# Kernel optimization log

Hardware: AMD Instinct MI355X
Metric: run time of the kernel (lower is better)

The kernel has to match this reference:

```python
import jax, jax.numpy as jnp
import numpy as np

B, N = 16, 16          # batch, boxes per image
H, W = 640, 640        # image size
PH, PW = 300, 300      # learned patch size
MIN_AREA = 60.0
MAX_ANG = 20.0 * np.pi / 180.0


def setup_inputs() -> dict:
    key = jax.random.key(0)
    k1, k2, k3 = jax.random.split(key, 3)
    images = jax.random.uniform(k1, (B, H, W, 3), jnp.float32, -1.0, 1.0)
    patch = jax.random.uniform(k2, (PH, PW, 3), jnp.float32, -1.0, 1.0)
    kb1, kb2, kb3 = jax.random.split(k3, 3)
    ymin = jax.random.uniform(kb1, (B, N), jnp.float32, 0.0, H - 220.0)
    xmin = jax.random.uniform(kb2, (B, N), jnp.float32, 0.0, W - 220.0)
    hw = jax.random.uniform(kb3, (B, N, 2), jnp.float32, 100.0, 200.0)
    boxes = jnp.stack([ymin, xmin, ymin + hw[..., 0], xmin + hw[..., 1]], axis=-1)
    scale = jnp.float32(0.4)
    return {"boxes": boxes, "images": images, "patch": patch, "scale": scale}


def _bilinear(img, ys, xs):
    # img [Ph,Pw,3]; ys,xs [H,W] continuous source coords -> [H,W,3]
    Ph, Pw = img.shape[0], img.shape[1]
    y0 = jnp.floor(ys)
    x0 = jnp.floor(xs)
    wy = (ys - y0)[..., None]
    wx = (xs - x0)[..., None]
    y0i = jnp.clip(y0.astype(jnp.int32), 0, Ph - 1)
    y1i = jnp.clip(y0i + 1, 0, Ph - 1)
    x0i = jnp.clip(x0.astype(jnp.int32), 0, Pw - 1)
    x1i = jnp.clip(x0i + 1, 0, Pw - 1)
    v00 = img[y0i, x0i]
    v01 = img[y0i, x1i]
    v10 = img[y1i, x0i]
    v11 = img[y1i, x1i]
    return v00 * (1 - wy) * (1 - wx) + v01 * (1 - wy) * wx + v10 * wy * (1 - wx) + v11 * wy * wx


def _per_image(img, boxes_i, patch, scale, key):
    # random_print_adjust: per-channel affine jitter of the patch
    kw, kb, kloop = jax.random.split(key, 3)
    w = jax.random.normal(kw, (1, 1, 3), jnp.float32) * 0.1 + 0.5
    b = jax.random.normal(kb, (1, 1, 3), jnp.float32) * 0.01
    p = jnp.clip(w * patch + b, -1.0, 1.0)
    # BrightnessMatcher: shift patch mean brightness to match the image
    p = jnp.clip(p + (jnp.mean(img) - jnp.mean(p)), -1.0, 1.0)

    oimg = img
    mask0 = jnp.zeros_like(img)
    yy, xx = jnp.meshgrid(jnp.arange(H, dtype=jnp.float32),
                          jnp.arange(W, dtype=jnp.float32), indexing="ij")

    def step(carry, inp):
        image, mask = carry
        box, kk = inp
        ymin, xmin, ymax, xmax = box[0], box[1], box[2], box[3]
        h = ymax - ymin
        ww = xmax - xmin
        longer = jnp.maximum(h, ww)
        ps = jnp.floor(longer * scale)                       # patch_h == patch_w
        diag = jnp.minimum(jnp.sqrt(2.0).astype(jnp.float32) * ps, jnp.float32(W))
        oy = ymin + h / 2.0
        ox = xmin + ww / 2.0
        y0 = jnp.maximum(oy - diag / 2.0, 0.0)
        x0 = jnp.maximum(ox - diag / 2.0, 0.0)
        y0 = jnp.where(y0 + diag > H, H - diag, y0)
        x0 = jnp.where(x0 + diag > W, W - diag, x0)
        # int casts as in the TF code (values are >= 0, trunc == floor)
        y0i = jnp.floor(y0)
        x0i = jnp.floor(x0)
        phi = jnp.maximum(jnp.floor(ps), 1.0)
        diagi = jnp.floor(diag)
        valid_box = (phi * phi) > MIN_AREA

        k1, k2, k3 = jax.random.split(kk, 3)
        angle = jax.random.uniform(k1, (), jnp.float32, -MAX_ANG, MAX_ANG)

        # inverse warp: output pixel -> padded-patch coords -> resized-patch coords
        u = yy - y0i
        v = xx - x0i
        in_sq = (u >= 0) & (v >= 0) & (u < diagi) & (v < diagi)
        c = (diagi - 1.0) / 2.0
        ca, sa = jnp.cos(angle), jnp.sin(angle)
        su = c + ca * (u - c) - sa * (v - c)
        sv = c + sa * (u - c) + ca * (v - c)
        top = jnp.floor((diagi - phi) / 2.0)   # pad offset (floor top/left)
        py = su - top
        px = sv - top
        valid_src = (py >= 0) & (py <= phi - 1) & (px >= 0) & (px <= phi - 1)
        # resized-patch coords -> original patch coords (bilinear resize, half-pixel)
        sy = (py + 0.5) * (PH / phi) - 0.5
        sx = (px + 0.5) * (PW / phi) - 0.5
        samp = _bilinear(p, sy, sx)                                   # [H,W,3]
        noise = jax.random.uniform(k2, samp.shape, jnp.float32, -0.1, 0.1)
        bright = jax.random.uniform(k3, (), jnp.float32, -0.3, 0.3)
        im = jnp.clip(samp + noise + bright, -1.0, 1.0)
        val = jnp.where(valid_src[..., None], im, -2.0)
        val = jnp.where(val < -1.0, image, val)   # fill with current background
        val = jnp.clip(val, -1.0, 1.0)
        sel = (in_sq & valid_box)[..., None]
        new_image = jnp.where(sel, val, image)
        new_mask = jnp.where(sel, oimg - val, mask)
        return (new_image, new_mask), None

    keys = jax.random.split(kloop, N)
    (img_out, mask_out), _ = jax.lax.scan(step, (img, mask0), (boxes_i, keys))
    return img_out, mask_out


def reference(boxes, images, patch, scale):
    keys = jax.random.split(jax.random.key(42), B)
    img_out, mask_out = jax.vmap(_per_image, in_axes=(0, 0, None, None, 0))(
        images, boxes, patch, scale, keys)
    return img_out, mask_out
```

## Files before the change

kernel.cpp:

```cpp
#include <hip/hip_runtime.h>
#include <stdint.h>
#include <math.h>

#define B_ 16
#define N_ 16
#define H_ 640
#define W_ 640
#define PH_ 300
#define PW_ 300

#define IMG_ELEMS (H_*W_*3)
#define PATCH_ELEMS (PH_*PW_*3)

#define TROWS 16
#define TCOLS 64
#define TILES_Y (H_/TROWS)
#define TILES_X (W_/TCOLS)
#define TILES_PER_IMG (TILES_Y*TILES_X)
#define NTILES (B_*TILES_PER_IMG)

typedef float f32x4 __attribute__((ext_vector_type(4)));

__device__ __forceinline__ uint2 tf2x32(uint32_t k0, uint32_t k1, uint32_t x0, uint32_t x1) {
  uint32_t k2 = k0 ^ k1 ^ 0x1BD11BDAu;
#define TFR(r) x0 += x1; x1 = (x1 << (r)) | (x1 >> (32 - (r))); x1 ^= x0;
  x0 += k0; x1 += k1;
  TFR(13) TFR(15) TFR(26) TFR(6)
  x0 += k1; x1 += k2 + 1u;
  TFR(17) TFR(29) TFR(16) TFR(24)
  x0 += k2; x1 += k0 + 2u;
  TFR(13) TFR(15) TFR(26) TFR(6)
  x0 += k0; x1 += k1 + 3u;
  TFR(17) TFR(29) TFR(16) TFR(24)
  x0 += k1; x1 += k2 + 4u;
  TFR(13) TFR(15) TFR(26) TFR(6)
  x0 += k2; x1 += k0 + 5u;
#undef TFR
  return make_uint2(x0, x1);
}

__device__ __forceinline__ uint32_t rb32(uint32_t k0, uint32_t k1, uint32_t i) {
  uint2 o = tf2x32(k0, k1, 0u, i);
  return o.x ^ o.y;
}

__device__ __forceinline__ float u01f(uint32_t bits) {
  return __uint_as_float((bits >> 9) | 0x3F800000u) - 1.0f;
}

__device__ __forceinline__ float erfinv32(float x) {
  float w = -log1pf(-x * x);
  float p;
  if (w < 5.0f) {
    w = w - 2.5f;
    p = 2.81022636e-08f;
    p = fmaf(p, w, 3.43273939e-07f);
    p = fmaf(p, w, -3.5233877e-06f);
    p = fmaf(p, w, -4.39150654e-06f);
    p = fmaf(p, w, 0.00021858087f);
    p = fmaf(p, w, -0.00125372503f);
    p = fmaf(p, w, -0.00417768164f);
    p = fmaf(p, w, 0.246640727f);
    p = fmaf(p, w, 1.50140941f);
  } else {
    w = sqrtf(w) - 3.0f;
    p = -0.000200214257f;
    p = fmaf(p, w, 0.000100950558f);
    p = fmaf(p, w, 0.00134934322f);
    p = fmaf(p, w, -0.00367342844f);
    p = fmaf(p, w, 0.00573950773f);
    p = fmaf(p, w, -0.0076224613f);
    p = fmaf(p, w, 0.00943887047f);
    p = fmaf(p, w, 1.00167406f);
    p = fmaf(p, w, 2.83297682f);
  }
  return p * x;
}

__device__ __forceinline__ float jnormal(uint32_t bits) {
  float lo = __uint_as_float(0xBF7FFFFFu);
  float span = 1.0f - lo;
  float u = fmaxf(lo, u01f(bits) * span + lo);
  return 1.4142135623730951f * erfinv32(u);
}

__global__ __launch_bounds__(256) void reduce_kernel(
    const float* __restrict__ images, const float* __restrict__ patch,
    double* __restrict__ partials) {
  int b = blockIdx.y, j = blockIdx.x, t = threadIdx.x;
  __shared__ float swb[6];
  if (t < 6) {
    uint2 kb  = tf2x32(0u, 42u, 0u, (uint32_t)b);
    uint2 kw  = tf2x32(kb.x, kb.y, 0u, 0u);
    uint2 kbk = tf2x32(kb.x, kb.y, 0u, 1u);
    swb[t] = (t < 3) ? (jnormal(rb32(kw.x,  kw.y,  (uint32_t)t)) * 0.1f + 0.5f)
                     : (jnormal(rb32(kbk.x, kbk.y, (uint32_t)(t - 3))) * 0.01f);
  }
  __syncthreads();
  const float* img = images + (size_t)b * IMG_ELEMS;
  double s = 0.0;
  for (int i = j * 256 + t; i < IMG_ELEMS; i += 64 * 256) s += (double)img[i];
  float w0 = swb[0], w1 = swb[1], w2 = swb[2];
  float b0 = swb[3], b1 = swb[4], b2 = swb[5];
  double sp = 0.0;
  for (int i = j * 256 + t; i < PATCH_ELEMS; i += 64 * 256) {
    int q = i / 3; int ch = i - q * 3;
    float wv = (ch == 0) ? w0 : ((ch == 1) ? w1 : w2);
    float bv = (ch == 0) ? b0 : ((ch == 1) ? b1 : b2);
    float pv = fminf(fmaxf(wv * patch[i] + bv, -1.0f), 1.0f);
    sp += (double)pv;
  }
  __shared__ double sh[256];
  sh[t] = s; __syncthreads();
  for (int o = 128; o > 0; o >>= 1) { if (t < o) sh[t] += sh[t + o]; __syncthreads(); }
  if (t == 0) partials[((size_t)b * 64 + j) * 2 + 0] = sh[0];
  __syncthreads();
  sh[t] = sp; __syncthreads();
  for (int o = 128; o > 0; o >>= 1) { if (t < o) sh[t] += sh[t + o]; __syncthreads(); }
  if (t == 0) partials[((size_t)b * 64 + j) * 2 + 1] = sh[0];
}

__global__ void setup_finalize_kernel(
    const float* __restrict__ boxes, const float* __restrict__ scale_p,
    const double* __restrict__ partials,
    float* __restrict__ params, float* __restrict__ wb, float* __restrict__ dvals) {
  int t = threadIdx.x;
  if (t < B_) {
    double si = 0.0, sp = 0.0;
    for (int j = 0; j < 64; j++) {
      si += partials[((size_t)t * 64 + j) * 2 + 0];
      sp += partials[((size_t)t * 64 + j) * 2 + 1];
    }
    float mi = (float)(si / (double)IMG_ELEMS);
    float mp = (float)(sp / (double)PATCH_ELEMS);
    dvals[t] = mi - mp;
  }
  if (t >= B_*N_) return;
  int b = t >> 4, n = t & 15;
  uint2 kb = tf2x32(0u, 42u, 0u, (uint32_t)b);
  uint2 kw  = tf2x32(kb.x, kb.y, 0u, 0u);
  uint2 kbk = tf2x32(kb.x, kb.y, 0u, 1u);
  uint2 kl  = tf2x32(kb.x, kb.y, 0u, 2u);
  if (n == 0) {
    wb[b*8+0] = jnormal(rb32(kw.x,  kw.y,  0u)) * 0.1f + 0.5f;
    wb[b*8+1] = jnormal(rb32(kw.x,  kw.y,  1u)) * 0.1f + 0.5f;
    wb[b*8+2] = jnormal(rb32(kw.x,  kw.y,  2u)) * 0.1f + 0.5f;
    wb[b*8+3] = jnormal(rb32(kbk.x, kbk.y, 0u)) * 0.01f;
    wb[b*8+4] = jnormal(rb32(kbk.x, kbk.y, 1u)) * 0.01f;
    wb[b*8+5] = jnormal(rb32(kbk.x, kbk.y, 2u)) * 0.01f;
  }
  uint2 kk = tf2x32(kl.x, kl.y, 0u, (uint32_t)n);
  uint2 k1 = tf2x32(kk.x, kk.y, 0u, 0u);
  uint2 k2 = tf2x32(kk.x, kk.y, 0u, 1u);
  uint2 k3 = tf2x32(kk.x, kk.y, 0u, 2u);
  const float MA = (float)(20.0 * 3.14159265358979323846 / 180.0);
  float angle  = fmaxf(-MA,   u01f(rb32(k1.x, k1.y, 0u)) * (MA - (-MA)) + (-MA));
  float bright = fmaxf(-0.3f, u01f(rb32(k3.x, k3.y, 0u)) * (0.3f - (-0.3f)) + (-0.3f));

  const float* bx = boxes + (size_t)t * 4;
  float ymin = bx[0], xmin = bx[1], ymax = bx[2], xmax = bx[3];
  float sc = scale_p[0];
  float h = ymax - ymin, ww = xmax - xmin;
  float longer = fmaxf(h, ww);
  float ps = floorf(longer * sc);
  float diag = fminf(sqrtf(2.0f) * ps, (float)W_);
  float oy = ymin + h * 0.5f;
  float ox = xmin + ww * 0.5f;
  float y0 = fmaxf(oy - diag * 0.5f, 0.0f);
  float x0 = fmaxf(ox - diag * 0.5f, 0.0f);
  if (y0 + diag > (float)H_) y0 = (float)H_ - diag;
  if (x0 + diag > (float)W_) x0 = (float)W_ - diag;
  float y0i = floorf(y0), x0i = floorf(x0);
  float phi = fmaxf(floorf(ps), 1.0f);
  float diagi = floorf(diag);
  float validf = ((phi * phi) > 60.0f) ? 1.0f : 0.0f;
  float c = (diagi - 1.0f) * 0.5f;
  float top = floorf((diagi - phi) * 0.5f);

  float* P = params + t * 16;
  P[0] = y0i; P[1] = x0i; P[2] = diagi; P[3] = phi;
  P[4] = c;
  P[5] = (float)cos((double)angle);
  P[6] = (float)sin((double)angle);
  P[7] = top;
  P[8] = bright; P[9] = (float)PH_ / phi; P[10] = 0.0f; P[11] = validf;
  P[12] = __uint_as_float(k2.x); P[13] = __uint_as_float(k2.y); P[14] = 0.0f; P[15] = 0.0f;
}

__global__ __launch_bounds__(256) void main_kernel(
    const float* __restrict__ images, const float* __restrict__ patch,
    const float* __restrict__ params, const float* __restrict__ wb,
    const float* __restrict__ dvals, float* __restrict__ out) {
  __shared__ float sP[N_ * 16];
  __shared__ float sWB[6];
  __shared__ int sList[N_];
  __shared__ int sCount;
  __shared__ float sT[TROWS * 192];

  int bid = blockIdx.x;
  int b  = (bid & 7) * 2 + ((bid >> 3) & 1);
  int tl = bid >> 4;
  int ty = tl / TILES_X;
  int tx = tl - ty * TILES_X;
  int tid = threadIdx.x;

  if (tid < N_ * 16) sP[tid] = params[b * N_ * 16 + tid];
  if (tid < 6) sWB[tid] = wb[b * 8 + tid];
  if (tid == 0) {
    const float* Pb = params + b * N_ * 16;
    float ys = (float)(ty * TROWS), ye = (float)(ty * TROWS + TROWS - 1);
    float xs = (float)(tx * TCOLS), xe = (float)(tx * TCOLS + TCOLS - 1);
    int cnt = 0;
    for (int n = 0; n < N_; n++) {
      const float* P = Pb + n * 16;
      if (P[11] == 0.0f) continue;
      float last = P[2] - 1.0f;
      if (P[0] + last < ys || P[0] > ye) continue;
      if (P[1] + last < xs || P[1] > xe) continue;
      sList[cnt++] = n;
    }
    sCount = cnt;
  }
  __syncthreads();

  int lane = tid & 63;
  int wv   = tid >> 6;
  size_t ibase = (size_t)b * IMG_ELEMS;
  size_t moff  = (size_t)B_ * IMG_ELEMS;

  int   ck[3], lrk[3];
  size_t fbk[3];
#pragma unroll
  for (int k = 0; k < 3; k++) {
    int t4 = k * 64 + lane;
    int r  = t4 / 48;
    int c  = t4 - r * 48;
    int lr = wv * 4 + r;
    ck[k] = c; lrk[k] = lr;
    fbk[k] = ibase + ((size_t)(ty * TROWS + lr) * W_ + tx * TCOLS) * 3 + (size_t)c * 4;
  }

  if (sCount == 0) {
    const f32x4 z = {0.0f, 0.0f, 0.0f, 0.0f};
#pragma unroll
    for (int k = 0; k < 3; k++) {
      f32x4 d = *(const f32x4*)(images + fbk[k]);
      *(f32x4*)(out + fbk[k]) = d;
      *(f32x4*)(out + moff + fbk[k]) = z;
    }
    return;
  }

  float dsh = dvals[b];

#pragma unroll
  for (int k = 0; k < 3; k++) {
    f32x4 d = *(const f32x4*)(images + fbk[k]);
    *(f32x4*)(&sT[lrk[k] * 192 + ck[k] * 4]) = d;
  }

  int   pj[4];  float yfj[4];
  float xf = (float)(tx * TCOLS + lane);
#pragma unroll
  for (int j = 0; j < 4; j++) {
    int row = ty * TROWS + wv * 4 + j;
    pj[j]  = row * W_ + tx * TCOLS + lane;
    yfj[j] = (float)row;
  }

  float orig[12], img[12], mkv[12];
#pragma unroll
  for (int j = 0; j < 4; j++) {
    int base = (wv * 4 + j) * 192 + lane * 3;
    orig[j*3+0] = sT[base + 0];
    orig[j*3+1] = sT[base + 1];
    orig[j*3+2] = sT[base + 2];
  }
#pragma unroll
  for (int e = 0; e < 12; e++) { img[e] = orig[e]; mkv[e] = 0.0f; }

  int cnt = sCount;
  for (int li = 0; li < cnt; li++) {
    const float* P = sP + sList[li] * 16;
    float P0 = P[0], P1 = P[1], diagi = P[2];
    float phi = P[3], c = P[4], ca = P[5], sa = P[6], top = P[7], bright = P[8], sph = P[9];
    uint32_t k2a = __float_as_uint(P[12]);
    uint32_t k2b = __float_as_uint(P[13]);
    float v = xf - P1;
    bool vok = (v >= 0.0f && v < diagi);
    float t2 = v - c;
#pragma unroll
    for (int j = 0; j < 4; j++) {
      float u = yfj[j] - P0;
      if (!(u >= 0.0f && u < diagi)) continue;
      if (!vok) continue;
      float t1 = u - c;
      float su = (c + ca * t1) - sa * t2;
      float sv = (c + sa * t1) + ca * t2;
      float py = su - top;
      float px = sv - top;
      bool vsrc = (py >= 0.0f) && (py <= phi - 1.0f) && (px >= 0.0f) && (px <= phi - 1.0f);
      if (vsrc) {
        float sy = (py + 0.5f) * sph - 0.5f;
        float sx = (px + 0.5f) * sph - 0.5f;
        float fy = floorf(sy), fx = floorf(sx);
        float wy = sy - fy, wxv = sx - fx;
        int iy0 = min(max((int)fy, 0), PH_ - 1);
        int iy1 = min(iy0 + 1, PH_ - 1);
        int ix0 = min(max((int)fx, 0), PW_ - 1);
        int ix1 = min(ix0 + 1, PW_ - 1);
        int o00 = (iy0 * PW_ + ix0) * 3;
        int o01 = (iy0 * PW_ + ix1) * 3;
        int o10 = (iy1 * PW_ + ix0) * 3;
        int o11 = (iy1 * PW_ + ix1) * 3;
        float omwy = 1.0f - wy, omwx = 1.0f - wxv;
        int nbase = pj[j] * 3;
#pragma unroll
        for (int ch = 0; ch < 3; ch++) {
          float wv2 = sWB[ch], bv = sWB[3 + ch];
          float a00 = fminf(fmaxf(wv2 * patch[o00 + ch] + bv, -1.0f), 1.0f);
          float a01 = fminf(fmaxf(wv2 * patch[o01 + ch] + bv, -1.0f), 1.0f);
          float a10 = fminf(fmaxf(wv2 * patch[o10 + ch] + bv, -1.0f), 1.0f);
          float a11 = fminf(fmaxf(wv2 * patch[o11 + ch] + bv, -1.0f), 1.0f);
          a00 = fminf(fmaxf(a00 + dsh, -1.0f), 1.0f);
          a01 = fminf(fmaxf(a01 + dsh, -1.0f), 1.0f);
          a10 = fminf(fmaxf(a10 + dsh, -1.0f), 1.0f);
          a11 = fminf(fmaxf(a11 + dsh, -1.0f), 1.0f);
          float samp = ((a00 * omwy) * omwx) + ((a01 * omwy) * wxv)
                     + ((a10 * wy) * omwx) + ((a11 * wy) * wxv);
          uint32_t bits = rb32(k2a, k2b, (uint32_t)(nbase + ch));
          float nz = fmaxf(-0.1f, u01f(bits) * (0.1f - (-0.1f)) + (-0.1f));
          float imv = fminf(fmaxf((samp + nz) + bright, -1.0f), 1.0f);
          img[j * 3 + ch] = imv;
          mkv[j * 3 + ch] = orig[j * 3 + ch] - imv;
        }
      } else {
#pragma unroll
        for (int ch = 0; ch < 3; ch++) mkv[j * 3 + ch] = orig[j * 3 + ch] - img[j * 3 + ch];
      }
    }
  }

#pragma unroll
  for (int j = 0; j < 4; j++) {
    int base = (wv * 4 + j) * 192 + lane * 3;
    sT[base + 0] = img[j*3+0];
    sT[base + 1] = img[j*3+1];
    sT[base + 2] = img[j*3+2];
  }
#pragma unroll
  for (int k = 0; k < 3; k++) {
    f32x4 d = *(const f32x4*)(&sT[lrk[k] * 192 + ck[k] * 4]);
    *(f32x4*)(out + fbk[k]) = d;
  }
#pragma unroll
  for (int j = 0; j < 4; j++) {
    int base = (wv * 4 + j) * 192 + lane * 3;
    sT[base + 0] = mkv[j*3+0];
    sT[base + 1] = mkv[j*3+1];
    sT[base + 2] = mkv[j*3+2];
  }
#pragma unroll
  for (int k = 0; k < 3; k++) {
    f32x4 d = *(const f32x4*)(&sT[lrk[k] * 192 + ck[k] * 4]);
    *(f32x4*)(out + moff + fbk[k]) = d;
  }
}

extern "C" void kernel_launch(void* const* d_in, const int* in_sizes, int n_in,
                              void* d_out, int out_size, void* d_ws, size_t ws_size,
                              hipStream_t stream) {
  const float* boxes  = (const float*)d_in[0];
  const float* images = (const float*)d_in[1];
  const float* patch  = (const float*)d_in[2];
  const float* scale  = (const float*)d_in[3];
  float* out = (float*)d_out;

  float* params = (float*)d_ws;
  float* wb     = params + B_ * N_ * 16;
  float* dvals  = wb + B_ * 8;
  double* partials = (double*)((char*)d_ws + 20480);

  reduce_kernel<<<dim3(64, B_), 256, 0, stream>>>(images, patch, partials);
  setup_finalize_kernel<<<1, 256, 0, stream>>>(boxes, scale, partials, params, wb, dvals);
  main_kernel<<<NTILES, 256, 0, stream>>>(images, patch, params, wb, dvals, out);
}
```

Before: 292.0 us.

## Make main kernel persistent and cull boxes per tile with a wave ballot

The main kernel now launches a fixed grid of 2048 blocks, and each block loops over tiles with a grid stride instead of handling exactly one tile. The stride is a multiple of 16, so a block keeps the same image and loads its parameters once. The serial per-tile box-overlap scan on thread 0, with its shared list, is replaced by a parallel test: each lane checks one box and a wave ballot builds a 16-bit overlap mask, which is walked with ctz. This removes the serial culling and block launch/setup overhead, at the cost of possible load imbalance because tiles differ in how many boxes touch them.

```diff
diff --git a/kernel.cpp b/kernel.cpp
--- a/kernel.cpp
+++ b/kernel.cpp
@@ -18,6 +18,7 @@
 #define TILES_X (W_/TCOLS)
 #define TILES_PER_IMG (TILES_Y*TILES_X)
 #define NTILES (B_*TILES_PER_IMG)
+#define MAIN_GRID 2048
 
 typedef float f32x4 __attribute__((ext_vector_type(4)));
 
@@ -193,177 +194,176 @@
     const float* __restrict__ dvals, float* __restrict__ out) {
   __shared__ float sP[N_ * 16];
   __shared__ float sWB[6];
-  __shared__ int sList[N_];
-  __shared__ int sCount;
   __shared__ float sT[TROWS * 192];
 
   int bid = blockIdx.x;
   int b  = (bid & 7) * 2 + ((bid >> 3) & 1);
-  int tl = bid >> 4;
-  int ty = tl / TILES_X;
-  int tx = tl - ty * TILES_X;
   int tid = threadIdx.x;
 
   if (tid < N_ * 16) sP[tid] = params[b * N_ * 16 + tid];
   if (tid < 6) sWB[tid] = wb[b * 8 + tid];
-  if (tid == 0) {
-    const float* Pb = params + b * N_ * 16;
-    float ys = (float)(ty * TROWS), ye = (float)(ty * TROWS + TROWS - 1);
-    float xs = (float)(tx * TCOLS), xe = (float)(tx * TCOLS + TCOLS - 1);
-    int cnt = 0;
-    for (int n = 0; n < N_; n++) {
-      const float* P = Pb + n * 16;
-      if (P[11] == 0.0f) continue;
-      float last = P[2] - 1.0f;
-      if (P[0] + last < ys || P[0] > ye) continue;
-      if (P[1] + last < xs || P[1] > xe) continue;
-      sList[cnt++] = n;
-    }
-    sCount = cnt;
-  }
   __syncthreads();
 
   int lane = tid & 63;
   int wv   = tid >> 6;
   size_t ibase = (size_t)b * IMG_ELEMS;
   size_t moff  = (size_t)B_ * IMG_ELEMS;
-
-  int   ck[3], lrk[3];
-  size_t fbk[3];
+  float dsh = dvals[b];
+
+  int ck[3], lrk[3];
 #pragma unroll
   for (int k = 0; k < 3; k++) {
     int t4 = k * 64 + lane;
     int r  = t4 / 48;
-    int c  = t4 - r * 48;
-    int lr = wv * 4 + r;
-    ck[k] = c; lrk[k] = lr;
-    fbk[k] = ibase + ((size_t)(ty * TROWS + lr) * W_ + tx * TCOLS) * 3 + (size_t)c * 4;
-  }
-
-  if (sCount == 0) {
-    const f32x4 z = {0.0f, 0.0f, 0.0f, 0.0f};
+    ck[k]  = t4 - r * 48;
+    lrk[k] = wv * 4 + r;
+  }
+
+  const float* Pc = sP + (tid & 15) * 16;
+  float cP0 = Pc[0], cP1 = Pc[1], cLast = Pc[2] - 1.0f;
+  bool cValid = (Pc[11] != 0.0f);
+
+  for (int g = bid; g < NTILES; g += MAIN_GRID) {
+    int tl = g >> 4;
+    int ty = tl / TILES_X;
+    int tx = tl - ty * TILES_X;
+
+    float ys = (float)(ty * TROWS), ye = ys + (float)(TROWS - 1);
+    float xs = (float)(tx * TCOLS), xe = xs + (float)(TCOLS - 1);
+    bool hit = cValid && !(cP0 + cLast < ys || cP0 > ye)
+                      && !(cP1 + cLast < xs || cP1 > xe);
+    uint32_t mask = (uint32_t)(__ballot(hit) & 0xFFFFull);
+
+    size_t fbk[3];
+#pragma unroll
+    for (int k = 0; k < 3; k++)
+      fbk[k] = ibase + ((size_t)(ty * TROWS + lrk[k]) * W_ + tx * TCOLS) * 3 + (size_t)ck[k] * 4;
+
+    if (mask == 0u) {
+      const f32x4 z = {0.0f, 0.0f, 0.0f, 0.0f};
+#pragma unroll
+      for (int k = 0; k < 3; k++) {
+        f32x4 d = *(const f32x4*)(images + fbk[k]);
+        *(f32x4*)(out + fbk[k]) = d;
+        *(f32x4*)(out + moff + fbk[k]) = z;
+      }
+      continue;
+    }
+
 #pragma unroll
     for (int k = 0; k < 3; k++) {
       f32x4 d = *(const f32x4*)(images + fbk[k]);
+      *(f32x4*)(&sT[lrk[k] * 192 + ck[k] * 4]) = d;
+    }
+
+    int   pj[4];  float yfj[4];
+    float xf = (float)(tx * TCOLS + lane);
+#pragma unroll
+    for (int j = 0; j < 4; j++) {
+      int row = ty * TROWS + wv * 4 + j;
+      pj[j]  = row * W_ + tx * TCOLS + lane;
+      yfj[j] = (float)row;
+    }
+
+    float orig[12], img[12], mkv[12];
+#pragma unroll
+    for (int j = 0; j < 4; j++) {
+      int base = (wv * 4 + j) * 192 + lane * 3;
+      orig[j*3+0] = sT[base + 0];
+      orig[j*3+1] = sT[base + 1];
+      orig[j*3+2] = sT[base + 2];
+    }
+#pragma unroll
+    for (int e = 0; e < 12; e++) { img[e] = orig[e]; mkv[e] = 0.0f; }
+
+    uint32_t m = mask;
+    while (m) {
+      int n = __builtin_ctz(m);
+      m &= m - 1u;
+      const float* P = sP + n * 16;
+      float P0 = P[0], P1 = P[1], diagi = P[2];
+      float phi = P[3], c = P[4], ca = P[5], sa = P[6], top = P[7], bright = P[8], sph = P[9];
+      uint32_t k2a = __float_as_uint(P[12]);
+      uint32_t k2b = __float_as_uint(P[13]);
+      float v = xf - P1;
+      bool vok = (v >= 0.0f && v < diagi);
+      float t2 = v - c;
+#pragma unroll
+      for (int j = 0; j < 4; j++) {
+        float u = yfj[j] - P0;
+        if (!(u >= 0.0f && u < diagi)) continue;
+        if (!vok) continue;
+        float t1 = u - c;
+        float su = (c + ca * t1) - sa * t2;
+        float sv = (c + sa * t1) + ca * t2;
+        float py = su - top;
+        float px = sv - top;
+        bool vsrc = (py >= 0.0f) && (py <= phi - 1.0f) && (px >= 0.0f) && (px <= phi - 1.0f);
+        if (vsrc) {
+          float sy = (py + 0.5f) * sph - 0.5f;
+          float sx = (px + 0.5f) * sph - 0.5f;
+          float fy = floorf(sy), fx = floorf(sx);
+          float wy = sy - fy, wxv = sx - fx;
+          int iy0 = min(max((int)fy, 0), PH_ - 1);
+          int iy1 = min(iy0 + 1, PH_ - 1);
+          int ix0 = min(max((int)fx, 0), PW_ - 1);
+          int ix1 = min(ix0 + 1, PW_ - 1);
+          int o00 = (iy0 * PW_ + ix0) * 3;
+          int o01 = (iy0 * PW_ + ix1) * 3;
+          int o10 = (iy1 * PW_ + ix0) * 3;
+          int o11 = (iy1 * PW_ + ix1) * 3;
+          float omwy = 1.0f - wy, omwx = 1.0f - wxv;
+          int nbase = pj[j] * 3;
+#pragma unroll
+          for (int ch = 0; ch < 3; ch++) {
+            float wv2 = sWB[ch], bv = sWB[3 + ch];
+            float a00 = fminf(fmaxf(wv2 * patch[o00 + ch] + bv, -1.0f), 1.0f);
+            float a01 = fminf(fmaxf(wv2 * patch[o01 + ch] + bv, -1.0f), 1.0f);
+            float a10 = fminf(fmaxf(wv2 * patch[o10 + ch] + bv, -1.0f), 1.0f);
+            float a11 = fminf(fmaxf(wv2 * patch[o11 + ch] + bv, -1.0f), 1.0f);
+            a00 = fminf(fmaxf(a00 + dsh, -1.0f), 1.0f);
+            a01 = fminf(fmaxf(a01 + dsh, -1.0f), 1.0f);
+            a10 = fminf(fmaxf(a10 + dsh, -1.0f), 1.0f);
+            a11 = fminf(fmaxf(a11 + dsh, -1.0f), 1.0f);
+            float samp = ((a00 * omwy) * omwx) + ((a01 * omwy) * wxv)
+                       + ((a10 * wy) * omwx) + ((a11 * wy) * wxv);
+            uint32_t bits = rb32(k2a, k2b, (uint32_t)(nbase + ch));
+            float nz = fmaxf(-0.1f, u01f(bits) * (0.1f - (-0.1f)) + (-0.1f));
+            float imv = fminf(fmaxf((samp + nz) + bright, -1.0f), 1.0f);
+            img[j * 3 + ch] = imv;
+            mkv[j * 3 + ch] = orig[j * 3 + ch] - imv;
+          }
+        } else {
+#pragma unroll
+          for (int ch = 0; ch < 3; ch++) mkv[j * 3 + ch] = orig[j * 3 + ch] - img[j * 3 + ch];
+        }
+      }
+    }
+
+#pragma unroll
+    for (int j = 0; j < 4; j++) {
+      int base = (wv * 4 + j) * 192 + lane * 3;
+      sT[base + 0] = img[j*3+0];
+      sT[base + 1] = img[j*3+1];
+      sT[base + 2] = img[j*3+2];
+    }
+#pragma unroll
+    for (int k = 0; k < 3; k++) {
+      f32x4 d = *(const f32x4*)(&sT[lrk[k] * 192 + ck[k] * 4]);
       *(f32x4*)(out + fbk[k]) = d;
-      *(f32x4*)(out + moff + fbk[k]) = z;
-    }
-    return;
-  }
-
-  float dsh = dvals[b];
-
-#pragma unroll
-  for (int k = 0; k < 3; k++) {
-    f32x4 d = *(const f32x4*)(images + fbk[k]);
-    *(f32x4*)(&sT[lrk[k] * 192 + ck[k] * 4]) = d;
-  }
-
-  int   pj[4];  float yfj[4];
-  float xf = (float)(tx * TCOLS + lane);
-#pragma unroll
-  for (int j = 0; j < 4; j++) {
-    int row = ty * TROWS + wv * 4 + j;
-    pj[j]  = row * W_ + tx * TCOLS + lane;
-    yfj[j] = (float)row;
-  }
-
-  float orig[12], img[12], mkv[12];
-#pragma unroll
-  for (int j = 0; j < 4; j++) {
-    int base = (wv * 4 + j) * 192 + lane * 3;
-    orig[j*3+0] = sT[base + 0];
-    orig[j*3+1] = sT[base + 1];
-    orig[j*3+2] = sT[base + 2];
-  }
-#pragma unroll
-  for (int e = 0; e < 12; e++) { img[e] = orig[e]; mkv[e] = 0.0f; }
-
-  int cnt = sCount;
-  for (int li = 0; li < cnt; li++) {
-    const float* P = sP + sList[li] * 16;
-    float P0 = P[0], P1 = P[1], diagi = P[2];
-    float phi = P[3], c = P[4], ca = P[5], sa = P[6], top = P[7], bright = P[8], sph = P[9];
-    uint32_t k2a = __float_as_uint(P[12]);
-    uint32_t k2b = __float_as_uint(P[13]);
-    float v = xf - P1;
-    bool vok = (v >= 0.0f && v < diagi);
-    float t2 = v - c;
+    }
 #pragma unroll
     for (int j = 0; j < 4; j++) {
-      float u = yfj[j] - P0;
-      if (!(u >= 0.0f && u < diagi)) continue;
-      if (!vok) continue;
-      float t1 = u - c;
-      float su = (c + ca * t1) - sa * t2;
-      float sv = (c + sa * t1) + ca * t2;
-      float py = su - top;
-      float px = sv - top;
-      bool vsrc = (py >= 0.0f) && (py <= phi - 1.0f) && (px >= 0.0f) && (px <= phi - 1.0f);
-      if (vsrc) {
-        float sy = (py + 0.5f) * sph - 0.5f;
-        float sx = (px + 0.5f) * sph - 0.5f;
-        float fy = floorf(sy), fx = floorf(sx);
-        float wy = sy - fy, wxv = sx - fx;
-        int iy0 = min(max((int)fy, 0), PH_ - 1);
-        int iy1 = min(iy0 + 1, PH_ - 1);
-        int ix0 = min(max((int)fx, 0), PW_ - 1);
-        int ix1 = min(ix0 + 1, PW_ - 1);
-        int o00 = (iy0 * PW_ + ix0) * 3;
-        int o01 = (iy0 * PW_ + ix1) * 3;
-        int o10 = (iy1 * PW_ + ix0) * 3;
-        int o11 = (iy1 * PW_ + ix1) * 3;
-        float omwy = 1.0f - wy, omwx = 1.0f - wxv;
-        int nbase = pj[j] * 3;
-#pragma unroll
-        for (int ch = 0; ch < 3; ch++) {
-          float wv2 = sWB[ch], bv = sWB[3 + ch];
-          float a00 = fminf(fmaxf(wv2 * patch[o00 + ch] + bv, -1.0f), 1.0f);
-          float a01 = fminf(fmaxf(wv2 * patch[o01 + ch] + bv, -1.0f), 1.0f);
-          float a10 = fminf(fmaxf(wv2 * patch[o10 + ch] + bv, -1.0f), 1.0f);
-          float a11 = fminf(fmaxf(wv2 * patch[o11 + ch] + bv, -1.0f), 1.0f);
-          a00 = fminf(fmaxf(a00 + dsh, -1.0f), 1.0f);
-          a01 = fminf(fmaxf(a01 + dsh, -1.0f), 1.0f);
-          a10 = fminf(fmaxf(a10 + dsh, -1.0f), 1.0f);
-          a11 = fminf(fmaxf(a11 + dsh, -1.0f), 1.0f);
-          float samp = ((a00 * omwy) * omwx) + ((a01 * omwy) * wxv)
-                     + ((a10 * wy) * omwx) + ((a11 * wy) * wxv);
-          uint32_t bits = rb32(k2a, k2b, (uint32_t)(nbase + ch));
-          float nz = fmaxf(-0.1f, u01f(bits) * (0.1f - (-0.1f)) + (-0.1f));
-          float imv = fminf(fmaxf((samp + nz) + bright, -1.0f), 1.0f);
-          img[j * 3 + ch] = imv;
-          mkv[j * 3 + ch] = orig[j * 3 + ch] - imv;
-        }
-      } else {
-#pragma unroll
-        for (int ch = 0; ch < 3; ch++) mkv[j * 3 + ch] = orig[j * 3 + ch] - img[j * 3 + ch];
-      }
-    }
-  }
-
-#pragma unroll
-  for (int j = 0; j < 4; j++) {
-    int base = (wv * 4 + j) * 192 + lane * 3;
-    sT[base + 0] = img[j*3+0];
-    sT[base + 1] = img[j*3+1];
-    sT[base + 2] = img[j*3+2];
-  }
-#pragma unroll
-  for (int k = 0; k < 3; k++) {
-    f32x4 d = *(const f32x4*)(&sT[lrk[k] * 192 + ck[k] * 4]);
-    *(f32x4*)(out + fbk[k]) = d;
-  }
-#pragma unroll
-  for (int j = 0; j < 4; j++) {
-    int base = (wv * 4 + j) * 192 + lane * 3;
-    sT[base + 0] = mkv[j*3+0];
-    sT[base + 1] = mkv[j*3+1];
-    sT[base + 2] = mkv[j*3+2];
-  }
-#pragma unroll
-  for (int k = 0; k < 3; k++) {
-    f32x4 d = *(const f32x4*)(&sT[lrk[k] * 192 + ck[k] * 4]);
-    *(f32x4*)(out + moff + fbk[k]) = d;
+      int base = (wv * 4 + j) * 192 + lane * 3;
+      sT[base + 0] = mkv[j*3+0];
+      sT[base + 1] = mkv[j*3+1];
+      sT[base + 2] = mkv[j*3+2];
+    }
+#pragma unroll
+    for (int k = 0; k < 3; k++) {
+      f32x4 d = *(const f32x4*)(&sT[lrk[k] * 192 + ck[k] * 4]);
+      *(f32x4*)(out + moff + fbk[k]) = d;
+    }
   }
 }
 
@@ -383,5 +383,5 @@
 
   reduce_kernel<<<dim3(64, B_), 256, 0, stream>>>(images, patch, partials);
   setup_finalize_kernel<<<1, 256, 0, stream>>>(boxes, scale, partials, params, wb, dvals);
-  main_kernel<<<NTILES, 256, 0, stream>>>(images, patch, params, wb, dvals, out);
-}
+  main_kernel<<<MAIN_GRID, 256, 0, stream>>>(images, patch, params, wb, dvals, out);
+}
```

Result: no change. 291.3 us (-0.2%).
